# Kernel optimization log

Hardware: AMD Instinct MI355X
Metric: run time of the kernel (lower is better)

Reference implementation:

```python
import jax, jax.numpy as jnp
import numpy as np

B, V, L, C, H = 2, 8, 256, 1024, 16

def setup_inputs() -> dict:
    key = jax.random.key(0)
    ks = jax.random.split(key, 6)
    s = 0.02  # init scale for weights
    x = jax.random.normal(ks[0], (B, V, L, C), jnp.float32)
    Wq = jax.random.normal(ks[1], (C, C), jnp.float32) * s
    Wk = jax.random.normal(ks[2], (C, C), jnp.float32) * s
    Wv = jax.random.normal(ks[3], (C, C), jnp.float32) * s
    Wp = jax.random.normal(ks[4], (C, C), jnp.float32) * s
    bp = jnp.zeros((C,), jnp.float32)
    return {"x": x, "Wq": Wq, "Wk": Wk, "Wv": Wv, "Wp": Wp, "bp": bp}

def _view_mask(V, L):
    # view-level allow mask, expanded to token level [S, S]
    vi = jnp.arange(V)
    qv, kv = vi[:, None], vi[None, :]
    cross = ((qv == 0) & (kv == 1)) | ((qv == 1) & (kv == 0))
    later = (qv > 1) | (kv > 1)
    allow = cross | (later & (qv >= kv))  # [V, V]
    return jnp.repeat(jnp.repeat(allow, L, axis=0), L, axis=1)  # [V*L, V*L]

def reference(x, Wq, Wk, Wv, Wp, bp):
    b, v, l, c = x.shape
    h = H
    dh = c // h
    scale = dh ** -0.5
    s = v * l
    xf = x.reshape(b, s, c)
    # torch Linear: y = x @ W.T
    q = (xf @ Wq.T).reshape(b, s, h, dh).transpose(0, 2, 1, 3)  # [b,h,s,dh]
    k = (xf @ Wk.T).reshape(b, s, h, dh).transpose(0, 2, 1, 3)
    vv = (xf @ Wv.T).reshape(b, s, h, dh).transpose(0, 2, 1, 3)
    scores = jnp.einsum('bhqd,bhkd->bhqk', q, k) * scale  # [b,h,s,s]
    mask = _view_mask(v, l)
    scores = jnp.where(mask, scores, -jnp.inf)
    attn = jax.nn.softmax(scores, axis=-1)
    out = jnp.einsum('bhqk,bhkd->bhqd', attn, vv)
    out = out.transpose(0, 2, 1, 3).reshape(b, v, l, c)
    return out @ Wp.T + bp
```

## Files before the change

kernel.cpp:

```cpp
#include <hip/hip_runtime.h>
#include <stdint.h>

typedef unsigned short ushort_t;
typedef __attribute__((ext_vector_type(8))) __bf16 bf16x8;
typedef __attribute__((ext_vector_type(4))) float floatx4;
typedef __attribute__((ext_vector_type(2))) uint32_t uint32x2;

__device__ __forceinline__ ushort_t f2bf(float f) {
    uint32_t u = __builtin_bit_cast(uint32_t, f);
    u += 0x7fffu + ((u >> 16) & 1u);
    return (ushort_t)(u >> 16);
}

typedef __attribute__((address_space(1))) const void glb_void;
typedef __attribute__((address_space(3))) void lds_void;
__device__ __forceinline__ void gld16(const void* g, void* l) {
    __builtin_amdgcn_global_load_lds((glb_void*)g, (lds_void*)l, 16, 0, 0);
}

#define QSCALE 0.18033688011112042f

__global__ void cast_kernel(const float* __restrict__ x,
                            const float* __restrict__ Wq, const float* __restrict__ Wk,
                            const float* __restrict__ Wv, const float* __restrict__ Wp,
                            ushort_t* __restrict__ xb, ushort_t* __restrict__ Wqkvb,
                            ushort_t* __restrict__ Wpb)
{
    const int64_t NX = 4194304, NW = 1048576;
    int64_t i4 = ((int64_t)blockIdx.x * blockDim.x + threadIdx.x) * 4;
    const float* src; ushort_t* dst; int64_t off;
    if (i4 < NX)            { src = x;  dst = xb;          off = i4; }
    else if (i4 < NX+NW)    { src = Wq; dst = Wqkvb;       off = i4 - NX; }
    else if (i4 < NX+2*NW)  { src = Wk; dst = Wqkvb + NW;  off = i4 - NX - NW; }
    else if (i4 < NX+3*NW)  { src = Wv; dst = Wqkvb + 2*NW;off = i4 - NX - 2*NW; }
    else                    { src = Wp; dst = Wpb;         off = i4 - NX - 3*NW; }
    float4 v = *(const float4*)(src + off);
    ushort4 o;
    o.x = f2bf(v.x); o.y = f2bf(v.y); o.z = f2bf(v.z); o.w = f2bf(v.w);
    *(ushort4*)(dst + off) = o;
}

#define BM 128
#define BN 128
#define BK 32

__global__ __launch_bounds__(256, 3)
void gemm_bt(const ushort_t* __restrict__ A, const ushort_t* __restrict__ Bmat,
             int M, int N, int K, int mode,
             ushort_t* __restrict__ qb, ushort_t* __restrict__ kb, ushort_t* __restrict__ vtb,
             float* __restrict__ outf, const float* __restrict__ bias)
{
    __shared__ ushort_t As[BM * BK];
    __shared__ ushort_t Bs[BN * BK];
    const int tid  = threadIdx.x;
    const int lane = tid & 63;
    const int wave = tid >> 6;
    const int m0 = blockIdx.x * BM;
    const int n0 = blockIdx.y * BN;
    const int wrow = (wave >> 1) * 64;
    const int wcol = (wave & 1) * 64;
    const int q_ = lane >> 4;
    const int ml = lane & 15;

    floatx4 acc[4][4];
    for (int i = 0; i < 4; i++) for (int j = 0; j < 4; j++) acc[i][j] = floatx4{0.f,0.f,0.f,0.f};

    const int t0 = wave * 2, t1 = wave * 2 + 1;
    const int row_l = lane >> 2;
    const int col_l = (lane & 3) * 8;
    const ushort_t* Ag0 = A    + (int64_t)(m0 + t0*16 + row_l) * K + col_l;
    const ushort_t* Ag1 = A    + (int64_t)(m0 + t1*16 + row_l) * K + col_l;
    const ushort_t* Bg0 = Bmat + (int64_t)(n0 + t0*16 + row_l) * K + col_l;
    const ushort_t* Bg1 = Bmat + (int64_t)(n0 + t1*16 + row_l) * K + col_l;
    ushort_t* Al0 = As + t0*512; ushort_t* Al1 = As + t1*512;
    ushort_t* Bl0 = Bs + t0*512; ushort_t* Bl1 = Bs + t1*512;

    for (int k0 = 0; k0 < K; k0 += BK) {
        __syncthreads();
        gld16(Ag0 + k0, Al0);
        gld16(Ag1 + k0, Al1);
        gld16(Bg0 + k0, Bl0);
        gld16(Bg1 + k0, Bl1);
        __syncthreads();
        bf16x8 af[4], bf[4];
        for (int mt = 0; mt < 4; mt++)
            af[mt] = *(const bf16x8*)(As + (wrow + mt*16 + ml) * BK + q_*8);
        for (int nt = 0; nt < 4; nt++)
            bf[nt] = *(const bf16x8*)(Bs + (wcol + nt*16 + ml) * BK + q_*8);
        for (int mt = 0; mt < 4; mt++)
            for (int nt = 0; nt < 4; nt++)
                acc[mt][nt] = __builtin_amdgcn_mfma_f32_16x16x32_bf16(af[mt], bf[nt], acc[mt][nt], 0, 0, 0);
    }

    if (mode == 0) {
        for (int mt = 0; mt < 4; mt++) for (int nt = 0; nt < 4; nt++) {
            floatx4 v = acc[mt][nt];
            int col = n0 + wcol + nt*16 + ml;
            int which = col >> 10;
            int nn = col & 1023;
            int h = nn >> 6, d = nn & 63;
            if (which < 2) {
                ushort_t* dst = (which == 0) ? qb : kb;
                float sc = (which == 0) ? QSCALE : 1.0f;
                for (int r = 0; r < 4; r++) {
                    int rowg = m0 + wrow + mt*16 + q_*4 + r;
                    int b = rowg >> 11, s = rowg & 2047;
                    dst[(((int64_t)(b*16 + h) * 2048 + s) << 6) + d] = f2bf(v[r] * sc);
                }
            } else {
                int rowg0 = m0 + wrow + mt*16 + q_*4;
                int b = rowg0 >> 11, sbase = rowg0 & 2047;
                ushort4 o;
                o.x = f2bf(v[0]); o.y = f2bf(v[1]); o.z = f2bf(v[2]); o.w = f2bf(v[3]);
                *(ushort4*)(vtb + (((int64_t)(b*16 + h) * 64 + d) << 11) + sbase) = o;
            }
        }
    } else {
        for (int mt = 0; mt < 4; mt++) for (int nt = 0; nt < 4; nt++) {
            floatx4 v = acc[mt][nt];
            int col = n0 + wcol + nt*16 + ml;
            float bv = bias[col];
            for (int r = 0; r < 4; r++) {
                int rowg = m0 + wrow + mt*16 + q_*4 + r;
                outf[(int64_t)rowg * N + col] = v[r] + bv;
            }
        }
    }
}

__global__ __launch_bounds__(128, 2)
void attn_kernel(const ushort_t* __restrict__ Q, const ushort_t* __restrict__ Kb,
                 const ushort_t* __restrict__ Vt, ushort_t* __restrict__ Out)
{
    __shared__ ushort_t Kd[2][8192];
    __shared__ ushort_t Vl[8192];
    __shared__ ushort_t Pl[2 * 32 * 136];

    int bi = blockIdx.x;
    int bh  = (bi & 7) + 8 * ((bi >> 3) & 3);
    int qt2 = (bi >> 5) & 3;
    int g8  = bi >> 7;
    int qv  = (g8 < 6) ? (7 - g8) : (g8 - 6);
    int b = bh >> 4, h = bh & 15;
    int tid = threadIdx.x;
    int wave = tid >> 6, lane = tid & 63;
    int q_ = lane >> 4, ml = lane & 15;
    int rlane = lane & 15, clane = lane >> 4;
    int s0 = qv*256 + qt2*64 + wave*32;

    const ushort_t* Kbh = Kb + ((int64_t)bh << 17);
    const ushort_t* Vbh = Vt + ((int64_t)bh << 17);
    ushort_t* Pw = Pl + wave * (32 * 136);

    const ushort_t* Qp = Q + (((int64_t)bh*2048 + s0 + ml) << 6) + q_*8;
    bf16x8 aq0A = *(const bf16x8*)(Qp);
    bf16x8 aq1A = *(const bf16x8*)(Qp + 32);
    bf16x8 aq0B = *(const bf16x8*)(Qp + 1024);
    bf16x8 aq1B = *(const bf16x8*)(Qp + 1024 + 32);

    floatx4 o_accA[4], o_accB[4];
    for (int i = 0; i < 4; i++) { o_accA[i] = floatx4{0.f,0.f,0.f,0.f};
                                  o_accB[i] = floatx4{0.f,0.f,0.f,0.f}; }
    float lsumA = 0.f, lsumB = 0.f;

    const int nviews = (qv < 2) ? 1 : (qv + 1);
    const int NT = nviews * 2;
    const int vfix = qv ^ 1;


    {
        int vw = (nviews == 1) ? vfix : 0;
        int koff = vw * 256;
        #pragma unroll
        for (int i = 0; i < 8; i++) {
            int id = wave*8 + i;
            const ushort_t* gk = Kbh + (((int64_t)(koff + (id >> 1)*16 + rlane)) << 6)
                                     + (id & 1)*32 + clane*8;
            gld16(gk, Kd[0] + id*512);
        }
        #pragma unroll
        for (int i = 0; i < 8; i++) {
            int id = wave*8 + i;
            const ushort_t* gv = Vbh + ((int64_t)((id & 3)*16 + rlane) << 11)
                                     + koff + (id >> 2)*32 + clane*8;
            gld16(gv, Vl + id*512);
        }
    }

    for (int t = 0; t < NT; ++t) {
        int cur = t & 1;
        int koff = ((nviews == 1) ? vfix : (t >> 1)) * 256 + (t & 1) * 128;

        if (t + 1 < NT) {
            int koff_n = ((nviews == 1) ? vfix : ((t + 1) >> 1)) * 256 + ((t + 1) & 1) * 128;
            #pragma unroll
            for (int i = 0; i < 8; i++) {
                int id = wave*8 + i;
                const ushort_t* gk = Kbh + (((int64_t)(koff_n + (id >> 1)*16 + rlane)) << 6)
                                         + (id & 1)*32 + clane*8;
                gld16(gk, Kd[cur ^ 1] + id*512);
            }
            asm volatile("s_waitcnt vmcnt(8)" ::: "memory");
        } else {
            asm volatile("s_waitcnt vmcnt(0)" ::: "memory");
        }
        __builtin_amdgcn_s_barrier();

        const ushort_t* Kl = Kd[cur];
        #pragma unroll
        for (int kt = 0; kt < 8; kt++) {
            bf16x8 k0 = *(const bf16x8*)(Kl + kt*1024 + lane*8);
            bf16x8 k1 = *(const bf16x8*)(Kl + kt*1024 + 512 + lane*8);
            floatx4 czA = floatx4{0.f,0.f,0.f,0.f};
            floatx4 czB = floatx4{0.f,0.f,0.f,0.f};
            __builtin_amdgcn_s_setprio(1);
            czA = __builtin_amdgcn_mfma_f32_16x16x32_bf16(k0, aq0A, czA, 0, 0, 0);
            czA = __builtin_amdgcn_mfma_f32_16x16x32_bf16(k1, aq1A, czA, 0, 0, 0);
            czB = __builtin_amdgcn_mfma_f32_16x16x32_bf16(k0, aq0B, czB, 0, 0, 0);
            czB = __builtin_amdgcn_mfma_f32_16x16x32_bf16(k1, aq1B, czB, 0, 0, 0);
            __builtin_amdgcn_s_setprio(0);

            float a0 = __builtin_amdgcn_exp2f(czA[0]);
            float a1 = __builtin_amdgcn_exp2f(czA[1]);
            float a2 = __builtin_amdgcn_exp2f(czA[2]);
            float a3 = __builtin_amdgcn_exp2f(czA[3]);
            lsumA += (a0 + a1) + (a2 + a3);
            uint32x2 wa;
            wa[0] = (uint32_t)f2bf(a0) | ((uint32_t)f2bf(a1) << 16);
            wa[1] = (uint32_t)f2bf(a2) | ((uint32_t)f2bf(a3) << 16);
            *(uint32x2*)(Pw + ml*136 + kt*16 + q_*4) = wa;

            float b0 = __builtin_amdgcn_exp2f(czB[0]);
            float b1 = __builtin_amdgcn_exp2f(czB[1]);
            float b2 = __builtin_amdgcn_exp2f(czB[2]);
            float b3 = __builtin_amdgcn_exp2f(czB[3]);
            lsumB += (b0 + b1) + (b2 + b3);
            uint32x2 wb;
            wb[0] = (uint32_t)f2bf(b0) | ((uint32_t)f2bf(b1) << 16);
            wb[1] = (uint32_t)f2bf(b2) | ((uint32_t)f2bf(b3) << 16);
            *(uint32x2*)(Pw + (16 + ml)*136 + kt*16 + q_*4) = wb;
        }

        asm volatile("s_waitcnt lgkmcnt(0)" ::: "memory");

        #pragma unroll
        for (int g = 0; g < 4; g++) {
            bf16x8 apA = *(const bf16x8*)(Pw + ml*136 + g*32 + q_*8);
            bf16x8 apB = *(const bf16x8*)(Pw + (16 + ml)*136 + g*32 + q_*8);
            __builtin_amdgcn_s_setprio(1);
            #pragma unroll
            for (int dt = 0; dt < 4; dt++) {
                bf16x8 vv = *(const bf16x8*)(Vl + (g*4 + dt)*512 + lane*8);
                o_accA[dt] = __builtin_amdgcn_mfma_f32_16x16x32_bf16(apA, vv, o_accA[dt], 0, 0, 0);
                o_accB[dt] = __builtin_amdgcn_mfma_f32_16x16x32_bf16(apB, vv, o_accB[dt], 0, 0, 0);
            }
            __builtin_amdgcn_s_setprio(0);
        }

        __builtin_amdgcn_s_barrier();

        if (t + 1 < NT) {
            int koff_n = ((nviews == 1) ? vfix : ((t + 1) >> 1)) * 256 + ((t + 1) & 1) * 128;
            #pragma unroll
            for (int i = 0; i < 8; i++) {
                int id = wave*8 + i;
                const ushort_t* gv = Vbh + ((int64_t)((id & 3)*16 + rlane) << 11)
                                         + koff_n + (id >> 2)*32 + clane*8;
                gld16(gv, Vl + id*512);
            }
        }
    }

    lsumA += __shfl_xor(lsumA, 16);
    lsumA += __shfl_xor(lsumA, 32);
    lsumB += __shfl_xor(lsumB, 16);
    lsumB += __shfl_xor(lsumB, 32);
    float rinvA[4], rinvB[4];
    #pragma unroll
    for (int r = 0; r < 4; r++) {
        rinvA[r] = 1.0f / __shfl(lsumA, q_*4 + r);
        rinvB[r] = 1.0f / __shfl(lsumB, q_*4 + r);
    }

    #pragma unroll
    for (int dt = 0; dt < 4; dt++)
        #pragma unroll
        for (int r = 0; r < 4; r++) {
            int srA = s0 + q_*4 + r;
            Out[((int64_t)b*2048 + srA) * 1024 + h*64 + dt*16 + ml] = f2bf(o_accA[dt][r] * rinvA[r]);
            int srB = s0 + 16 + q_*4 + r;
            Out[((int64_t)b*2048 + srB) * 1024 + h*64 + dt*16 + ml] = f2bf(o_accB[dt][r] * rinvB[r]);
        }
}

extern "C" void kernel_launch(void* const* d_in, const int* in_sizes, int n_in,
                              void* d_out, int out_size, void* d_ws, size_t ws_size,
                              hipStream_t stream) {
    const float* x  = (const float*)d_in[0];
    const float* Wq = (const float*)d_in[1];
    const float* Wk = (const float*)d_in[2];
    const float* Wv = (const float*)d_in[3];
    const float* Wp = (const float*)d_in[4];
    const float* bp = (const float*)d_in[5];
    float* out = (float*)d_out;

    char* ws = (char*)d_ws;
    ushort_t* xb    = (ushort_t*)(ws);
    ushort_t* Wqkvb = (ushort_t*)(ws + ((size_t)8  << 20));
    ushort_t* Wpb   = (ushort_t*)(ws + ((size_t)14 << 20));
    ushort_t* qb    = (ushort_t*)(ws + ((size_t)16 << 20));
    ushort_t* kbuf  = (ushort_t*)(ws + ((size_t)24 << 20));
    ushort_t* vtb   = (ushort_t*)(ws + ((size_t)40 << 20));
    ushort_t* attno = xb;

    cast_kernel<<<8192, 256, 0, stream>>>(x, Wq, Wk, Wv, Wp, xb, Wqkvb, Wpb);

    dim3 g0(4096 / BM, 3072 / BN);
    gemm_bt<<<g0, 256, 0, stream>>>(xb, Wqkvb, 4096, 3072, 1024, 0,
                                    qb, kbuf, vtb, nullptr, nullptr);

    attn_kernel<<<1024, 128, 0, stream>>>(qb, kbuf, vtb, attno);

    dim3 g1(4096 / BM, 1024 / BN);
    gemm_bt<<<g1, 256, 0, stream>>>(attno, Wpb, 4096, 1024, 1024, 1,
                                    nullptr, nullptr, nullptr, out, bp);
}
```

Baseline: 200.3 us.

## Use 4-wave attention blocks sharing K/V tiles and halve per-wave P staging

Each attention block now has four waves covering 128 query rows instead of two waves covering 64, so each K/V tile staged in LDS is reused by twice as many queries. Half as many blocks are launched, and each wave issues half as many async global-to-LDS loads. The per-wave P scratch shrinks to 16 rows: the B-half probabilities are held in registers and written to LDS only after the A-half PV MFMAs finish, which serialises the two halves. This cuts LDS footprint and K/V traffic but adds register pressure and an extra LDS round-trip and wait per tile.

```diff
diff --git a/kernel.cpp b/kernel.cpp
--- a/kernel.cpp
+++ b/kernel.cpp
@@ -128,29 +128,29 @@
     }
 }
 
-__global__ __launch_bounds__(128, 2)
+__global__ __launch_bounds__(256, 2)
 void attn_kernel(const ushort_t* __restrict__ Q, const ushort_t* __restrict__ Kb,
                  const ushort_t* __restrict__ Vt, ushort_t* __restrict__ Out)
 {
     __shared__ ushort_t Kd[2][8192];
     __shared__ ushort_t Vl[8192];
-    __shared__ ushort_t Pl[2 * 32 * 136];
+    __shared__ ushort_t Pl[4 * 16 * 136];
 
     int bi = blockIdx.x;
-    int bh  = (bi & 7) + 8 * ((bi >> 3) & 3);
-    int qt2 = (bi >> 5) & 3;
-    int g8  = bi >> 7;
-    int qv  = (g8 < 6) ? (7 - g8) : (g8 - 6);
+    int bh = (bi & 7) + 8 * ((bi >> 3) & 3);
+    int qt = (bi >> 5) & 1;
+    int g8 = bi >> 6;
+    int qv = (g8 < 4) ? (7 - g8) : (g8 - 4);
     int b = bh >> 4, h = bh & 15;
     int tid = threadIdx.x;
     int wave = tid >> 6, lane = tid & 63;
     int q_ = lane >> 4, ml = lane & 15;
     int rlane = lane & 15, clane = lane >> 4;
-    int s0 = qv*256 + qt2*64 + wave*32;
+    int s0 = qv*256 + qt*128 + wave*32;
 
     const ushort_t* Kbh = Kb + ((int64_t)bh << 17);
     const ushort_t* Vbh = Vt + ((int64_t)bh << 17);
-    ushort_t* Pw = Pl + wave * (32 * 136);
+    ushort_t* Pw = Pl + wave * (16 * 136);
 
     const ushort_t* Qp = Q + (((int64_t)bh*2048 + s0 + ml) << 6) + q_*8;
     bf16x8 aq0A = *(const bf16x8*)(Qp);
@@ -169,18 +169,17 @@
 
 
     {
-        int vw = (nviews == 1) ? vfix : 0;
-        int koff = vw * 256;
-        #pragma unroll
-        for (int i = 0; i < 8; i++) {
-            int id = wave*8 + i;
+        int koff = ((nviews == 1) ? vfix : 0) * 256;
+        #pragma unroll
+        for (int i = 0; i < 4; i++) {
+            int id = wave*4 + i;
             const ushort_t* gk = Kbh + (((int64_t)(koff + (id >> 1)*16 + rlane)) << 6)
                                      + (id & 1)*32 + clane*8;
             gld16(gk, Kd[0] + id*512);
         }
         #pragma unroll
-        for (int i = 0; i < 8; i++) {
-            int id = wave*8 + i;
+        for (int i = 0; i < 4; i++) {
+            int id = wave*4 + i;
             const ushort_t* gv = Vbh + ((int64_t)((id & 3)*16 + rlane) << 11)
                                      + koff + (id >> 2)*32 + clane*8;
             gld16(gv, Vl + id*512);
@@ -189,24 +188,24 @@
 
     for (int t = 0; t < NT; ++t) {
         int cur = t & 1;
-        int koff = ((nviews == 1) ? vfix : (t >> 1)) * 256 + (t & 1) * 128;
 
         if (t + 1 < NT) {
             int koff_n = ((nviews == 1) ? vfix : ((t + 1) >> 1)) * 256 + ((t + 1) & 1) * 128;
             #pragma unroll
-            for (int i = 0; i < 8; i++) {
-                int id = wave*8 + i;
+            for (int i = 0; i < 4; i++) {
+                int id = wave*4 + i;
                 const ushort_t* gk = Kbh + (((int64_t)(koff_n + (id >> 1)*16 + rlane)) << 6)
                                          + (id & 1)*32 + clane*8;
                 gld16(gk, Kd[cur ^ 1] + id*512);
             }
-            asm volatile("s_waitcnt vmcnt(8)" ::: "memory");
+            asm volatile("s_waitcnt vmcnt(4)" ::: "memory");
         } else {
             asm volatile("s_waitcnt vmcnt(0)" ::: "memory");
         }
         __builtin_amdgcn_s_barrier();
 
         const ushort_t* Kl = Kd[cur];
+        uint32_t pb[16];
         #pragma unroll
         for (int kt = 0; kt < 8; kt++) {
             bf16x8 k0 = *(const bf16x8*)(Kl + kt*1024 + lane*8);
@@ -235,10 +234,8 @@
             float b2 = __builtin_amdgcn_exp2f(czB[2]);
             float b3 = __builtin_amdgcn_exp2f(czB[3]);
             lsumB += (b0 + b1) + (b2 + b3);
-            uint32x2 wb;
-            wb[0] = (uint32_t)f2bf(b0) | ((uint32_t)f2bf(b1) << 16);
-            wb[1] = (uint32_t)f2bf(b2) | ((uint32_t)f2bf(b3) << 16);
-            *(uint32x2*)(Pw + (16 + ml)*136 + kt*16 + q_*4) = wb;
+            pb[kt*2    ] = (uint32_t)f2bf(b0) | ((uint32_t)f2bf(b1) << 16);
+            pb[kt*2 + 1] = (uint32_t)f2bf(b2) | ((uint32_t)f2bf(b3) << 16);
         }
 
         asm volatile("s_waitcnt lgkmcnt(0)" ::: "memory");
@@ -246,12 +243,29 @@
         #pragma unroll
         for (int g = 0; g < 4; g++) {
             bf16x8 apA = *(const bf16x8*)(Pw + ml*136 + g*32 + q_*8);
-            bf16x8 apB = *(const bf16x8*)(Pw + (16 + ml)*136 + g*32 + q_*8);
             __builtin_amdgcn_s_setprio(1);
             #pragma unroll
             for (int dt = 0; dt < 4; dt++) {
                 bf16x8 vv = *(const bf16x8*)(Vl + (g*4 + dt)*512 + lane*8);
                 o_accA[dt] = __builtin_amdgcn_mfma_f32_16x16x32_bf16(apA, vv, o_accA[dt], 0, 0, 0);
+            }
+            __builtin_amdgcn_s_setprio(0);
+        }
+
+        #pragma unroll
+        for (int kt = 0; kt < 8; kt++) {
+            uint32x2 wb; wb[0] = pb[kt*2]; wb[1] = pb[kt*2 + 1];
+            *(uint32x2*)(Pw + ml*136 + kt*16 + q_*4) = wb;
+        }
+        asm volatile("s_waitcnt lgkmcnt(0)" ::: "memory");
+
+        #pragma unroll
+        for (int g = 0; g < 4; g++) {
+            bf16x8 apB = *(const bf16x8*)(Pw + ml*136 + g*32 + q_*8);
+            __builtin_amdgcn_s_setprio(1);
+            #pragma unroll
+            for (int dt = 0; dt < 4; dt++) {
+                bf16x8 vv = *(const bf16x8*)(Vl + (g*4 + dt)*512 + lane*8);
                 o_accB[dt] = __builtin_amdgcn_mfma_f32_16x16x32_bf16(apB, vv, o_accB[dt], 0, 0, 0);
             }
             __builtin_amdgcn_s_setprio(0);
@@ -262,8 +276,8 @@
         if (t + 1 < NT) {
             int koff_n = ((nviews == 1) ? vfix : ((t + 1) >> 1)) * 256 + ((t + 1) & 1) * 128;
             #pragma unroll
-            for (int i = 0; i < 8; i++) {
-                int id = wave*8 + i;
+            for (int i = 0; i < 4; i++) {
+                int id = wave*4 + i;
                 const ushort_t* gv = Vbh + ((int64_t)((id & 3)*16 + rlane) << 11)
                                          + koff_n + (id >> 2)*32 + clane*8;
                 gld16(gv, Vl + id*512);
@@ -319,7 +333,7 @@
     gemm_bt<<<g0, 256, 0, stream>>>(xb, Wqkvb, 4096, 3072, 1024, 0,
                                     qb, kbuf, vtb, nullptr, nullptr);
 
-    attn_kernel<<<1024, 128, 0, stream>>>(qb, kbuf, vtb, attno);
+    attn_kernel<<<512, 256, 0, stream>>>(qb, kbuf, vtb, attno);
 
     dim3 g1(4096 / BM, 1024 / BN);
     gemm_bt<<<g1, 256, 0, stream>>>(attno, Wpb, 4096, 1024, 1024, 1,
```

After: 192.5 us. 3.9% less time.
